# Kernel tuning notes

Hardware: AMD Instinct MI355X
Metric: run time of the kernel (lower is better)

## Reference

```python
import jax, jax.numpy as jnp
import numpy as np

N, XDIM, FACTOR, INTDIM = 1_000_000, 32, 2, 8
HID = XDIM * FACTOR  # 64


def setup_inputs() -> dict:
    key = jax.random.key(0)
    k1, k2, k3, k4, k5, k6 = jax.random.split(key, 6)
    edge_attr3 = jax.random.normal(k1, (N, XDIM), dtype=jnp.float32)
    edge_attr3_old = jax.random.randint(k2, (N, INTDIM), 0, 2).astype(jnp.int32)
    # kaiming-like uniform init (init distribution does not affect reference math)
    bw0 = 1.0 / np.sqrt(XDIM)
    w0 = jax.random.uniform(k3, (INTDIM, XDIM, HID), jnp.float32, -bw0, bw0)
    b0 = jax.random.uniform(k4, (INTDIM, HID), jnp.float32, -bw0, bw0)
    bw1 = 1.0 / np.sqrt(HID)
    w1 = jax.random.uniform(k5, (INTDIM, HID, 1), jnp.float32, -bw1, bw1)
    b1 = jax.random.uniform(k6, (INTDIM, 1), jnp.float32, -bw1, bw1)
    return {"edge_attr3": edge_attr3, "edge_attr3_old": edge_attr3_old,
            "w0": w0, "b0": b0, "w1": w1, "b1": b1}


def reference(edge_attr3, edge_attr3_old, w0, b0, w1, b1):
    # layer 0: per-head GEMM + bias + ReLU -> [n, d, q]
    h = jax.nn.relu(jnp.einsum('np,dpq->ndq', edge_attr3, w0) + b0)
    # layer 1: per-head projection to scalar, then squeeze -> [n, d]
    out = jnp.einsum('ndp,dp->nd', h, w1[:, :, 0]) + b1[:, 0]
    # boolean-mask gather (eager; dynamic output length as in torch out[mask])
    flat_idx = jnp.flatnonzero(edge_attr3_old.astype(bool))
    return out.reshape(-1)[flat_idx]
```

## Files before the change

### kernel.cpp

```cpp
#include <hip/hip_runtime.h>

#define NROWS 1000000
#define NB    3907
#define NT    62500
#define TPB   4
#define NBATCH (NT / TPB)
#define MLP_BLOCKS 1024

typedef __bf16 bf16x8 __attribute__((ext_vector_type(8)));
typedef float  f32x4  __attribute__((ext_vector_type(4)));

__device__ __forceinline__ unsigned cvt_pk_bf16(float lo, float hi) {
  unsigned r;
  asm("v_cvt_pk_bf16_f32 %0, %1, %2" : "=v"(r) : "v"(lo), "v"(hi));
  return r;
}

__global__ __launch_bounds__(256) void count_kernel(
    const int* __restrict__ mask, int* __restrict__ bsum) {
  int tid = threadIdx.x;
  int row = blockIdx.x * 256 + tid;
  int cnt = 0;
  if (row < NROWS) {
    const int4* mp = (const int4*)(mask + (long)row * 8);
    int4 a = mp[0], b = mp[1];
    cnt = (a.x != 0) + (a.y != 0) + (a.z != 0) + (a.w != 0) +
          (b.x != 0) + (b.y != 0) + (b.z != 0) + (b.w != 0);
  }
#pragma unroll
  for (int off = 1; off < 64; off <<= 1) cnt += __shfl_xor(cnt, off);
  __shared__ int ws[4];
  if ((tid & 63) == 0) ws[tid >> 6] = cnt;
  __syncthreads();
  if (tid == 0) bsum[blockIdx.x] = ws[0] + ws[1] + ws[2] + ws[3];
}

__global__ __launch_bounds__(1024) void scan_kernel(
    const int* __restrict__ bsum, int* __restrict__ boff) {
  __shared__ int lds[1024];
  int t = threadIdx.x;
  int i0 = t * 4;
  int c0 = (i0 + 0 < NB) ? bsum[i0 + 0] : 0;
  int c1 = (i0 + 1 < NB) ? bsum[i0 + 1] : 0;
  int c2 = (i0 + 2 < NB) ? bsum[i0 + 2] : 0;
  int c3 = (i0 + 3 < NB) ? bsum[i0 + 3] : 0;
  int s = c0 + c1 + c2 + c3;
  lds[t] = s;
  __syncthreads();
  for (int off = 1; off < 1024; off <<= 1) {
    int v = lds[t];
    int add = (t >= off) ? lds[t - off] : 0;
    __syncthreads();
    lds[t] = v + add;
    __syncthreads();
  }
  int excl = lds[t] - s;
  if (i0 + 0 < NB) boff[i0 + 0] = excl;
  excl += c0;
  if (i0 + 1 < NB) boff[i0 + 1] = excl;
  excl += c1;
  if (i0 + 2 < NB) boff[i0 + 2] = excl;
  excl += c2;
  if (i0 + 3 < NB) boff[i0 + 3] = excl;
}

__global__ __launch_bounds__(256) void expand_kernel(
    const int* __restrict__ mask, const int* __restrict__ boff,
    int* __restrict__ rowinfo) {
  int tid = threadIdx.x;
  int row = blockIdx.x * 256 + tid;
  bool valid = row < NROWS;
  unsigned mb = 0;
  int cnt = 0;
  if (valid) {
    const int4* mp = (const int4*)(mask + (long)row * 8);
    int4 a = mp[0], b = mp[1];
    mb = (unsigned)((a.x != 0) | ((a.y != 0) << 1) | ((a.z != 0) << 2) |
                    ((a.w != 0) << 3) | ((b.x != 0) << 4) | ((b.y != 0) << 5) |
                    ((b.z != 0) << 6) | ((b.w != 0) << 7));
    cnt = __popc(mb);
  }
  int incl = cnt;
#pragma unroll
  for (int off = 1; off < 64; off <<= 1) {
    int v = __shfl_up(incl, off);
    if ((tid & 63) >= off) incl += v;
  }
  __shared__ int wsum[4];
  if ((tid & 63) == 63) wsum[tid >> 6] = incl;
  __syncthreads();
  int w = tid >> 6;
  int wo = 0;
  if (w > 0) wo += wsum[0];
  if (w > 1) wo += wsum[1];
  if (w > 2) wo += wsum[2];
  int pos = boff[blockIdx.x] + wo + (incl - cnt);
  if (valid) rowinfo[row] = (pos << 8) | (int)mb;
}

__global__ __launch_bounds__(256, 2) void mlp_kernel(
    const float* __restrict__ x, const float* __restrict__ w0,
    const float* __restrict__ b0, const float* __restrict__ w1,
    const float* __restrict__ b1, const int* __restrict__ rowinfo,
    float* __restrict__ out) {
  __shared__ __bf16 sA[32 * 64 * 8];
  __shared__ float sB0[512];

  int tid = threadIdx.x;

#pragma unroll
  for (int i = 0; i < 8; ++i) {
    int fi = i * 256 + tid;
    int frag = fi >> 6;
    int lane = fi & 63;
    int d = frag >> 2, qb = frag & 3;
    int q = qb * 16 + (lane & 15);
    int kb = (lane >> 4) * 8;
    bf16x8 v;
#pragma unroll
    for (int j = 0; j < 8; ++j)
      v[j] = (__bf16)w0[d * 2048 + (kb + j) * 64 + q];
    *(bf16x8*)&sA[fi * 8] = v;
  }
  if (tid < 128) *(float4*)&sB0[tid * 4] = *(const float4*)&b0[tid * 4];
  __syncthreads();

  int l = tid & 63;
  int n = l & 15;
  int g = l >> 4;

  bf16x8 w1A, w1B;
  bool ownrow = (n < 8);
#pragma unroll
  for (int j = 0; j < 8; ++j) {
    int off = (j >> 2) * 16 + g * 4 + (j & 3);
    w1A[j] = ownrow ? (__bf16)w1[n * 64 + off]      : (__bf16)0.f;
    w1B[j] = ownrow ? (__bf16)w1[n * 64 + 32 + off] : (__bf16)0.f;
  }
  int4 w1Ai = *(int4*)&w1A;
  int4 w1Bi = *(int4*)&w1B;
  f32x4 b1C;
#pragma unroll
  for (int r = 0; r < 4; ++r) b1C[r] = b1[(g * 4 + r) & 7];

  int w = tid >> 6;
  int wv = blockIdx.x * 4 + w;
  const int W = MLP_BLOCKS * 4;

  for (int b = wv; b < NBATCH; b += W) {
    int t0 = b * TPB;

    bf16x8 xf0, xf1, xf2, xf3;
    {
      const float* xp;
      float4 a, c;
      uint4 ui;
#define LOADX(T, DST)                                              \
      xp = x + (long)((t0 + T) * 16 + n) * 32 + g * 8;             \
      a = *(const float4*)xp; c = *(const float4*)(xp + 4);        \
      ui.x = cvt_pk_bf16(a.x, a.y); ui.y = cvt_pk_bf16(a.z, a.w); \
      ui.z = cvt_pk_bf16(c.x, c.y); ui.w = cvt_pk_bf16(c.z, c.w); \
      DST = *(bf16x8*)&ui;
      LOADX(0, xf0) LOADX(1, xf1) LOADX(2, xf2) LOADX(3, xf3)
#undef LOADX
    }

    f32x4 O0 = b1C, O1 = b1C, O2 = b1C, O3 = b1C;

#pragma unroll 1
    for (int cp = 0; cp < 8; ++cp) {
      bool own = (n == cp);
      int4 z4 = {0, 0, 0, 0};
      int4 A2ai = own ? w1Ai : z4;
      int4 A2bi = own ? w1Bi : z4;
      bf16x8 A2a = *(bf16x8*)&A2ai;
      bf16x8 A2b = *(bf16x8*)&A2bi;
      int fb = cp * 4;
      bf16x8 Aw0 = *(const bf16x8*)&sA[(fb + 0) * 512 + l * 8];
      bf16x8 Aw1 = *(const bf16x8*)&sA[(fb + 1) * 512 + l * 8];
      bf16x8 Aw2 = *(const bf16x8*)&sA[(fb + 2) * 512 + l * 8];
      bf16x8 Aw3 = *(const bf16x8*)&sA[(fb + 3) * 512 + l * 8];
      f32x4 C0 = *(const f32x4*)&sB0[(fb + 0) * 16 + g * 4];
      f32x4 C1 = *(const f32x4*)&sB0[(fb + 1) * 16 + g * 4];
      f32x4 C2 = *(const f32x4*)&sB0[(fb + 2) * 16 + g * 4];
      f32x4 C3 = *(const f32x4*)&sB0[(fb + 3) * 16 + g * 4];

#define TILE(XF, OD) {                                                        \
      f32x4 Da = __builtin_amdgcn_mfma_f32_16x16x32_bf16(Aw0, XF, C0, 0,0,0); \
      f32x4 Db = __builtin_amdgcn_mfma_f32_16x16x32_bf16(Aw1, XF, C1, 0,0,0); \
      uint4 bu;                                                               \
      bu.x = cvt_pk_bf16(fmaxf(Da[0], 0.f), fmaxf(Da[1], 0.f));               \
      bu.y = cvt_pk_bf16(fmaxf(Da[2], 0.f), fmaxf(Da[3], 0.f));               \
      bu.z = cvt_pk_bf16(fmaxf(Db[0], 0.f), fmaxf(Db[1], 0.f));               \
      bu.w = cvt_pk_bf16(fmaxf(Db[2], 0.f), fmaxf(Db[3], 0.f));               \
      bf16x8 B2 = *(bf16x8*)&bu;                                              \
      OD = __builtin_amdgcn_mfma_f32_16x16x32_bf16(A2a, B2, OD, 0, 0, 0);     \
      f32x4 Dc = __builtin_amdgcn_mfma_f32_16x16x32_bf16(Aw2, XF, C2, 0,0,0); \
      f32x4 Dd = __builtin_amdgcn_mfma_f32_16x16x32_bf16(Aw3, XF, C3, 0,0,0); \
      bu.x = cvt_pk_bf16(fmaxf(Dc[0], 0.f), fmaxf(Dc[1], 0.f));               \
      bu.y = cvt_pk_bf16(fmaxf(Dc[2], 0.f), fmaxf(Dc[3], 0.f));               \
      bu.z = cvt_pk_bf16(fmaxf(Dd[0], 0.f), fmaxf(Dd[1], 0.f));               \
      bu.w = cvt_pk_bf16(fmaxf(Dd[2], 0.f), fmaxf(Dd[3], 0.f));               \
      bf16x8 B3 = *(bf16x8*)&bu;                                              \
      OD = __builtin_amdgcn_mfma_f32_16x16x32_bf16(A2b, B3, OD, 0, 0, 0); }
      TILE(xf0, O0) TILE(xf1, O1) TILE(xf2, O2) TILE(xf3, O3)
#undef TILE
    }

    if (g < 2) {
#define EPI(T, OD) {                                                     \
      int row = (t0 + T) * 16 + n;                                       \
      int info = rowinfo[row];                                           \
      unsigned mb = (unsigned)info & 255u;                               \
      int pos = (int)(((unsigned)info) >> 8) +                           \
                (g ? __popc(mb & 0xFu) : 0);                             \
      unsigned nib = (mb >> (g * 4)) & 0xFu;                             \
      if (nib & 1u) { out[pos] = OD[0]; pos++; }                         \
      if (nib & 2u) { out[pos] = OD[1]; pos++; }                         \
      if (nib & 4u) { out[pos] = OD[2]; pos++; }                         \
      if (nib & 8u) { out[pos] = OD[3]; }                                }
      EPI(0, O0) EPI(1, O1) EPI(2, O2) EPI(3, O3)
#undef EPI
    }
  }
}

extern "C" void kernel_launch(void* const* d_in, const int* in_sizes, int n_in,
                              void* d_out, int out_size, void* d_ws, size_t ws_size,
                              hipStream_t stream) {
  const float* x    = (const float*)d_in[0];
  const int*   mask = (const int*)d_in[1];
  const float* w0   = (const float*)d_in[2];
  const float* b0   = (const float*)d_in[3];
  const float* w1   = (const float*)d_in[4];
  const float* b1   = (const float*)d_in[5];
  float* out = (float*)d_out;

  int* bsum    = (int*)d_ws;
  int* boff    = bsum + NB;
  int* rowinfo = boff + NB;

  count_kernel<<<NB, 256, 0, stream>>>(mask, bsum);
  scan_kernel<<<1, 1024, 0, stream>>>(bsum, boff);
  expand_kernel<<<NB, 256, 0, stream>>>(mask, boff, rowinfo);
  mlp_kernel<<<MLP_BLOCKS, 256, 0, stream>>>(x, w0, b0, w1, b1, rowinfo, out);
}
```

Before: 92.25 us.

## Prefetch next batch of x, double-buffer LDS weight fragments, split accumulators

The MLP kernel now loads the next batch's x rows into registers while the current batch computes. It also double-buffers the per-head weight and bias fragments read from LDS across a loop unrolled by two, and splits the second-layer accumulation into two independent MFMA chains that are summed before the scatter. The block count is halved so each wave handles more batches and amortises the prefetch. The aim is to hide global and LDS latency and shorten MFMA dependency chains, at the cost of more registers and fewer resident waves.

```diff
diff --git a/kernel.cpp b/kernel.cpp
--- a/kernel.cpp
+++ b/kernel.cpp
@@ -5,7 +5,8 @@
 #define NT    62500
 #define TPB   4
 #define NBATCH (NT / TPB)
-#define MLP_BLOCKS 1024
+#define MLP_BLOCKS 512
+#define MLP_WAVES (MLP_BLOCKS * 4)
 
 typedef __bf16 bf16x8 __attribute__((ext_vector_type(8)));
 typedef float  f32x4  __attribute__((ext_vector_type(4)));
@@ -107,7 +108,6 @@
   __shared__ float sB0[512];
 
   int tid = threadIdx.x;
-
 #pragma unroll
   for (int i = 0; i < 8; ++i) {
     int fi = i * 256 + tid;
@@ -145,69 +145,122 @@
 
   int w = tid >> 6;
   int wv = blockIdx.x * 4 + w;
-  const int W = MLP_BLOCKS * 4;
+  const int W = MLP_WAVES;
+
+  float4 xa0, xa1, xa2, xa3, xa4, xa5, xa6, xa7;
+  {
+    const float* xp0 = x + (long)((wv * TPB + 0) * 16 + n) * 32 + g * 8;
+    const float* xp1 = x + (long)((wv * TPB + 1) * 16 + n) * 32 + g * 8;
+    const float* xp2 = x + (long)((wv * TPB + 2) * 16 + n) * 32 + g * 8;
+    const float* xp3 = x + (long)((wv * TPB + 3) * 16 + n) * 32 + g * 8;
+    xa0 = *(const float4*)xp0; xa1 = *(const float4*)(xp0 + 4);
+    xa2 = *(const float4*)xp1; xa3 = *(const float4*)(xp1 + 4);
+    xa4 = *(const float4*)xp2; xa5 = *(const float4*)(xp2 + 4);
+    xa6 = *(const float4*)xp3; xa7 = *(const float4*)(xp3 + 4);
+  }
 
   for (int b = wv; b < NBATCH; b += W) {
     int t0 = b * TPB;
 
     bf16x8 xf0, xf1, xf2, xf3;
     {
-      const float* xp;
-      float4 a, c;
       uint4 ui;
-#define LOADX(T, DST)                                              \
-      xp = x + (long)((t0 + T) * 16 + n) * 32 + g * 8;             \
-      a = *(const float4*)xp; c = *(const float4*)(xp + 4);        \
-      ui.x = cvt_pk_bf16(a.x, a.y); ui.y = cvt_pk_bf16(a.z, a.w); \
-      ui.z = cvt_pk_bf16(c.x, c.y); ui.w = cvt_pk_bf16(c.z, c.w); \
+#define CVTX(P, Q, DST)                                            \
+      ui.x = cvt_pk_bf16(P.x, P.y); ui.y = cvt_pk_bf16(P.z, P.w);  \
+      ui.z = cvt_pk_bf16(Q.x, Q.y); ui.w = cvt_pk_bf16(Q.z, Q.w);  \
       DST = *(bf16x8*)&ui;
-      LOADX(0, xf0) LOADX(1, xf1) LOADX(2, xf2) LOADX(3, xf3)
-#undef LOADX
-    }
-
-    f32x4 O0 = b1C, O1 = b1C, O2 = b1C, O3 = b1C;
-
-#pragma unroll 1
-    for (int cp = 0; cp < 8; ++cp) {
-      bool own = (n == cp);
-      int4 z4 = {0, 0, 0, 0};
-      int4 A2ai = own ? w1Ai : z4;
-      int4 A2bi = own ? w1Bi : z4;
-      bf16x8 A2a = *(bf16x8*)&A2ai;
-      bf16x8 A2b = *(bf16x8*)&A2bi;
-      int fb = cp * 4;
-      bf16x8 Aw0 = *(const bf16x8*)&sA[(fb + 0) * 512 + l * 8];
-      bf16x8 Aw1 = *(const bf16x8*)&sA[(fb + 1) * 512 + l * 8];
-      bf16x8 Aw2 = *(const bf16x8*)&sA[(fb + 2) * 512 + l * 8];
-      bf16x8 Aw3 = *(const bf16x8*)&sA[(fb + 3) * 512 + l * 8];
-      f32x4 C0 = *(const f32x4*)&sB0[(fb + 0) * 16 + g * 4];
-      f32x4 C1 = *(const f32x4*)&sB0[(fb + 1) * 16 + g * 4];
-      f32x4 C2 = *(const f32x4*)&sB0[(fb + 2) * 16 + g * 4];
-      f32x4 C3 = *(const f32x4*)&sB0[(fb + 3) * 16 + g * 4];
-
-#define TILE(XF, OD) {                                                        \
-      f32x4 Da = __builtin_amdgcn_mfma_f32_16x16x32_bf16(Aw0, XF, C0, 0,0,0); \
-      f32x4 Db = __builtin_amdgcn_mfma_f32_16x16x32_bf16(Aw1, XF, C1, 0,0,0); \
+      CVTX(xa0, xa1, xf0) CVTX(xa2, xa3, xf1)
+      CVTX(xa4, xa5, xf2) CVTX(xa6, xa7, xf3)
+#undef CVTX
+    }
+
+    {
+      int bn = b + W;
+      if (bn >= NBATCH) bn = b;
+      const float* yp0 = x + (long)((bn * TPB + 0) * 16 + n) * 32 + g * 8;
+      const float* yp1 = x + (long)((bn * TPB + 1) * 16 + n) * 32 + g * 8;
+      const float* yp2 = x + (long)((bn * TPB + 2) * 16 + n) * 32 + g * 8;
+      const float* yp3 = x + (long)((bn * TPB + 3) * 16 + n) * 32 + g * 8;
+      xa0 = *(const float4*)yp0; xa1 = *(const float4*)(yp0 + 4);
+      xa2 = *(const float4*)yp1; xa3 = *(const float4*)(yp1 + 4);
+      xa4 = *(const float4*)yp2; xa5 = *(const float4*)(yp2 + 4);
+      xa6 = *(const float4*)yp3; xa7 = *(const float4*)(yp3 + 4);
+    }
+
+    f32x4 Oa0 = b1C, Oa1 = b1C, Oa2 = b1C, Oa3 = b1C;
+    f32x4 Ob0 = {0.f, 0.f, 0.f, 0.f}, Ob1 = Ob0, Ob2 = Ob0, Ob3 = Ob0;
+
+    bf16x8 fA0 = *(const bf16x8*)&sA[0 * 512 + l * 8];
+    bf16x8 fA1 = *(const bf16x8*)&sA[1 * 512 + l * 8];
+    bf16x8 fA2 = *(const bf16x8*)&sA[2 * 512 + l * 8];
+    bf16x8 fA3 = *(const bf16x8*)&sA[3 * 512 + l * 8];
+    f32x4 cA0 = *(const f32x4*)&sB0[0 * 16 + g * 4];
+    f32x4 cA1 = *(const f32x4*)&sB0[1 * 16 + g * 4];
+    f32x4 cA2 = *(const f32x4*)&sB0[2 * 16 + g * 4];
+    f32x4 cA3 = *(const f32x4*)&sB0[3 * 16 + g * 4];
+
+#define COMPUTE(CP, F0, F1, F2, F3, C0v, C1v, C2v, C3v)                       \
+    {                                                                         \
+      bool own = (n == (CP));                                                 \
+      int4 z4 = {0, 0, 0, 0};                                                 \
+      int4 A2ai = own ? w1Ai : z4;                                            \
+      int4 A2bi = own ? w1Bi : z4;                                            \
+      bf16x8 A2a = *(bf16x8*)&A2ai;                                           \
+      bf16x8 A2b = *(bf16x8*)&A2bi;                                           \
+      TILE(xf0, F0, F1, F2, F3, C0v, C1v, C2v, C3v, Oa0, Ob0)                 \
+      TILE(xf1, F0, F1, F2, F3, C0v, C1v, C2v, C3v, Oa1, Ob1)                 \
+      TILE(xf2, F0, F1, F2, F3, C0v, C1v, C2v, C3v, Oa2, Ob2)                 \
+      TILE(xf3, F0, F1, F2, F3, C0v, C1v, C2v, C3v, Oa3, Ob3)                 \
+    }
+#define TILE(XF, F0, F1, F2, F3, C0v, C1v, C2v, C3v, OA, OB) {                \
+      f32x4 Da = __builtin_amdgcn_mfma_f32_16x16x32_bf16(F0, XF, C0v, 0,0,0); \
+      f32x4 Db = __builtin_amdgcn_mfma_f32_16x16x32_bf16(F1, XF, C1v, 0,0,0); \
       uint4 bu;                                                               \
       bu.x = cvt_pk_bf16(fmaxf(Da[0], 0.f), fmaxf(Da[1], 0.f));               \
       bu.y = cvt_pk_bf16(fmaxf(Da[2], 0.f), fmaxf(Da[3], 0.f));               \
       bu.z = cvt_pk_bf16(fmaxf(Db[0], 0.f), fmaxf(Db[1], 0.f));               \
       bu.w = cvt_pk_bf16(fmaxf(Db[2], 0.f), fmaxf(Db[3], 0.f));               \
       bf16x8 B2 = *(bf16x8*)&bu;                                              \
-      OD = __builtin_amdgcn_mfma_f32_16x16x32_bf16(A2a, B2, OD, 0, 0, 0);     \
-      f32x4 Dc = __builtin_amdgcn_mfma_f32_16x16x32_bf16(Aw2, XF, C2, 0,0,0); \
-      f32x4 Dd = __builtin_amdgcn_mfma_f32_16x16x32_bf16(Aw3, XF, C3, 0,0,0); \
+      OA = __builtin_amdgcn_mfma_f32_16x16x32_bf16(A2a, B2, OA, 0, 0, 0);     \
+      f32x4 Dc = __builtin_amdgcn_mfma_f32_16x16x32_bf16(F2, XF, C2v, 0,0,0); \
+      f32x4 Dd = __builtin_amdgcn_mfma_f32_16x16x32_bf16(F3, XF, C3v, 0,0,0); \
       bu.x = cvt_pk_bf16(fmaxf(Dc[0], 0.f), fmaxf(Dc[1], 0.f));               \
       bu.y = cvt_pk_bf16(fmaxf(Dc[2], 0.f), fmaxf(Dc[3], 0.f));               \
       bu.z = cvt_pk_bf16(fmaxf(Dd[0], 0.f), fmaxf(Dd[1], 0.f));               \
       bu.w = cvt_pk_bf16(fmaxf(Dd[2], 0.f), fmaxf(Dd[3], 0.f));               \
       bf16x8 B3 = *(bf16x8*)&bu;                                              \
-      OD = __builtin_amdgcn_mfma_f32_16x16x32_bf16(A2b, B3, OD, 0, 0, 0); }
-      TILE(xf0, O0) TILE(xf1, O1) TILE(xf2, O2) TILE(xf3, O3)
+      OB = __builtin_amdgcn_mfma_f32_16x16x32_bf16(A2b, B3, OB, 0, 0, 0); }
+
+#pragma unroll 1
+    for (int pp = 0; pp < 4; ++pp) {
+      int cpA = pp * 2, cpB = pp * 2 + 1;
+      int cpN = (pp * 2 + 2) & 7;
+      int fbB = cpB * 4, fbN = cpN * 4;
+      bf16x8 fB0 = *(const bf16x8*)&sA[(fbB + 0) * 512 + l * 8];
+      bf16x8 fB1 = *(const bf16x8*)&sA[(fbB + 1) * 512 + l * 8];
+      bf16x8 fB2 = *(const bf16x8*)&sA[(fbB + 2) * 512 + l * 8];
+      bf16x8 fB3 = *(const bf16x8*)&sA[(fbB + 3) * 512 + l * 8];
+      f32x4 cB0 = *(const f32x4*)&sB0[(fbB + 0) * 16 + g * 4];
+      f32x4 cB1 = *(const f32x4*)&sB0[(fbB + 1) * 16 + g * 4];
+      f32x4 cB2 = *(const f32x4*)&sB0[(fbB + 2) * 16 + g * 4];
+      f32x4 cB3 = *(const f32x4*)&sB0[(fbB + 3) * 16 + g * 4];
+      COMPUTE(cpA, fA0, fA1, fA2, fA3, cA0, cA1, cA2, cA3)
+      fA0 = *(const bf16x8*)&sA[(fbN + 0) * 512 + l * 8];
+      fA1 = *(const bf16x8*)&sA[(fbN + 1) * 512 + l * 8];
+      fA2 = *(const bf16x8*)&sA[(fbN + 2) * 512 + l * 8];
+      fA3 = *(const bf16x8*)&sA[(fbN + 3) * 512 + l * 8];
+      cA0 = *(const f32x4*)&sB0[(fbN + 0) * 16 + g * 4];
+      cA1 = *(const f32x4*)&sB0[(fbN + 1) * 16 + g * 4];
+      cA2 = *(const f32x4*)&sB0[(fbN + 2) * 16 + g * 4];
+      cA3 = *(const f32x4*)&sB0[(fbN + 3) * 16 + g * 4];
+      COMPUTE(cpB, fB0, fB1, fB2, fB3, cB0, cB1, cB2, cB3)
+    }
 #undef TILE
-    }
+#undef COMPUTE
 
     if (g < 2) {
+      f32x4 Os0 = Oa0 + Ob0, Os1 = Oa1 + Ob1;
+      f32x4 Os2 = Oa2 + Ob2, Os3 = Oa3 + Ob3;
 #define EPI(T, OD) {                                                     \
       int row = (t0 + T) * 16 + n;                                       \
       int info = rowinfo[row];                                           \
@@ -219,7 +272,7 @@
       if (nib & 2u) { out[pos] = OD[1]; pos++; }                         \
       if (nib & 4u) { out[pos] = OD[2]; pos++; }                         \
       if (nib & 8u) { out[pos] = OD[3]; }                                }
-      EPI(0, O0) EPI(1, O1) EPI(2, O2) EPI(3, O3)
+      EPI(0, Os0) EPI(1, Os1) EPI(2, Os2) EPI(3, Os3)
 #undef EPI
     }
   }
```

After: 95.59 us. 1.04x slower.

## Assign one head per wave with register-resident weights in 512-thread blocks

Applied to the files above, without the earlier changes.

Reorganizes the MLP kernel so each of eight waves in a 512-thread block handles one head for a shared group of four row tiles. Each wave keeps that head's W0 fragments, bias and W1 in registers, removing the LDS weight staging and the per-head loop. Each wave writes only its head's masked output directly. In exchange, every wave reloads and converts the same x tiles, multiplying x read requests by eight, which relies on cache hits.

```diff
diff --git a/kernel.cpp b/kernel.cpp
--- a/kernel.cpp
+++ b/kernel.cpp
@@ -3,9 +3,8 @@
 #define NROWS 1000000
 #define NB    3907
 #define NT    62500
-#define TPB   4
-#define NBATCH (NT / TPB)
-#define MLP_BLOCKS 1024
+#define GROUPS 15625
+#define MLP_BLOCKS 512
 
 typedef __bf16 bf16x8 __attribute__((ext_vector_type(8)));
 typedef float  f32x4  __attribute__((ext_vector_type(4)));
@@ -98,57 +97,51 @@
   if (valid) rowinfo[row] = (pos << 8) | (int)mb;
 }
 
-__global__ __launch_bounds__(256, 2) void mlp_kernel(
+__global__ __launch_bounds__(512, 4) void mlp_kernel(
     const float* __restrict__ x, const float* __restrict__ w0,
     const float* __restrict__ b0, const float* __restrict__ w1,
     const float* __restrict__ b1, const int* __restrict__ rowinfo,
     float* __restrict__ out) {
-  __shared__ __bf16 sA[32 * 64 * 8];
-  __shared__ float sB0[512];
-
   int tid = threadIdx.x;
-
-#pragma unroll
-  for (int i = 0; i < 8; ++i) {
-    int fi = i * 256 + tid;
-    int frag = fi >> 6;
-    int lane = fi & 63;
-    int d = frag >> 2, qb = frag & 3;
-    int q = qb * 16 + (lane & 15);
-    int kb = (lane >> 4) * 8;
-    bf16x8 v;
-#pragma unroll
-    for (int j = 0; j < 8; ++j)
-      v[j] = (__bf16)w0[d * 2048 + (kb + j) * 64 + q];
-    *(bf16x8*)&sA[fi * 8] = v;
-  }
-  if (tid < 128) *(float4*)&sB0[tid * 4] = *(const float4*)&b0[tid * 4];
-  __syncthreads();
-
+  int hp = tid >> 6;
   int l = tid & 63;
   int n = l & 15;
   int g = l >> 4;
 
-  bf16x8 w1A, w1B;
-  bool ownrow = (n < 8);
+  bf16x8 A0f, A1f, A2f, A3f;
+#define LDA(QB, DST) {                                              \
+    const float* wp = w0 + hp * 2048 + (g * 8) * 64 + QB * 16 + n;  \
+    _Pragma("unroll")                                               \
+    for (int j = 0; j < 8; ++j) DST[j] = (__bf16)wp[j * 64];        }
+  LDA(0, A0f) LDA(1, A1f) LDA(2, A2f) LDA(3, A3f)
+#undef LDA
+  f32x4 C0 = *(const f32x4*)&b0[hp * 64 + 0 * 16 + g * 4];
+  f32x4 C1 = *(const f32x4*)&b0[hp * 64 + 1 * 16 + g * 4];
+  f32x4 C2 = *(const f32x4*)&b0[hp * 64 + 2 * 16 + g * 4];
+  f32x4 C3 = *(const f32x4*)&b0[hp * 64 + 3 * 16 + g * 4];
+  bf16x8 w1a, w1b;
 #pragma unroll
   for (int j = 0; j < 8; ++j) {
     int off = (j >> 2) * 16 + g * 4 + (j & 3);
-    w1A[j] = ownrow ? (__bf16)w1[n * 64 + off]      : (__bf16)0.f;
-    w1B[j] = ownrow ? (__bf16)w1[n * 64 + 32 + off] : (__bf16)0.f;
-  }
-  int4 w1Ai = *(int4*)&w1A;
-  int4 w1Bi = *(int4*)&w1B;
+    w1a[j] = (__bf16)w1[hp * 64 + off];
+    w1b[j] = (__bf16)w1[hp * 64 + 32 + off];
+  }
+  bool own = (n == hp);
+  int4 z4 = {0, 0, 0, 0};
+  int4 tAa = own ? *(int4*)&w1a : z4;
+  int4 tAb = own ? *(int4*)&w1b : z4;
+  bf16x8 A2a = *(bf16x8*)&tAa;
+  bf16x8 A2b = *(bf16x8*)&tAb;
   f32x4 b1C;
 #pragma unroll
   for (int r = 0; r < 4; ++r) b1C[r] = b1[(g * 4 + r) & 7];
 
-  int w = tid >> 6;
-  int wv = blockIdx.x * 4 + w;
-  const int W = MLP_BLOCKS * 4;
-
-  for (int b = wv; b < NBATCH; b += W) {
-    int t0 = b * TPB;
+  int sg = hp >> 2;
+  int sr = hp & 3;
+  unsigned dmask = (1u << hp) - 1u;
+
+  for (int gq = blockIdx.x; gq < GROUPS; gq += MLP_BLOCKS) {
+    int t0 = gq * 4;
 
     bf16x8 xf0, xf1, xf2, xf3;
     {
@@ -158,70 +151,46 @@
 #define LOADX(T, DST)                                              \
       xp = x + (long)((t0 + T) * 16 + n) * 32 + g * 8;             \
       a = *(const float4*)xp; c = *(const float4*)(xp + 4);        \
-      ui.x = cvt_pk_bf16(a.x, a.y); ui.y = cvt_pk_bf16(a.z, a.w); \
-      ui.z = cvt_pk_bf16(c.x, c.y); ui.w = cvt_pk_bf16(c.z, c.w); \
+      ui.x = cvt_pk_bf16(a.x, a.y); ui.y = cvt_pk_bf16(a.z, a.w);  \
+      ui.z = cvt_pk_bf16(c.x, c.y); ui.w = cvt_pk_bf16(c.z, c.w);  \
       DST = *(bf16x8*)&ui;
       LOADX(0, xf0) LOADX(1, xf1) LOADX(2, xf2) LOADX(3, xf3)
 #undef LOADX
     }
 
-    f32x4 O0 = b1C, O1 = b1C, O2 = b1C, O3 = b1C;
-
-#pragma unroll 1
-    for (int cp = 0; cp < 8; ++cp) {
-      bool own = (n == cp);
-      int4 z4 = {0, 0, 0, 0};
-      int4 A2ai = own ? w1Ai : z4;
-      int4 A2bi = own ? w1Bi : z4;
-      bf16x8 A2a = *(bf16x8*)&A2ai;
-      bf16x8 A2b = *(bf16x8*)&A2bi;
-      int fb = cp * 4;
-      bf16x8 Aw0 = *(const bf16x8*)&sA[(fb + 0) * 512 + l * 8];
-      bf16x8 Aw1 = *(const bf16x8*)&sA[(fb + 1) * 512 + l * 8];
-      bf16x8 Aw2 = *(const bf16x8*)&sA[(fb + 2) * 512 + l * 8];
-      bf16x8 Aw3 = *(const bf16x8*)&sA[(fb + 3) * 512 + l * 8];
-      f32x4 C0 = *(const f32x4*)&sB0[(fb + 0) * 16 + g * 4];
-      f32x4 C1 = *(const f32x4*)&sB0[(fb + 1) * 16 + g * 4];
-      f32x4 C2 = *(const f32x4*)&sB0[(fb + 2) * 16 + g * 4];
-      f32x4 C3 = *(const f32x4*)&sB0[(fb + 3) * 16 + g * 4];
-
-#define TILE(XF, OD) {                                                        \
-      f32x4 Da = __builtin_amdgcn_mfma_f32_16x16x32_bf16(Aw0, XF, C0, 0,0,0); \
-      f32x4 Db = __builtin_amdgcn_mfma_f32_16x16x32_bf16(Aw1, XF, C1, 0,0,0); \
+#define TILE(T, XF) {                                                         \
+      f32x4 D0 = __builtin_amdgcn_mfma_f32_16x16x32_bf16(A0f, XF, C0, 0,0,0); \
+      f32x4 D1 = __builtin_amdgcn_mfma_f32_16x16x32_bf16(A1f, XF, C1, 0,0,0); \
+      f32x4 D2 = __builtin_amdgcn_mfma_f32_16x16x32_bf16(A2f, XF, C2, 0,0,0); \
+      f32x4 D3 = __builtin_amdgcn_mfma_f32_16x16x32_bf16(A3f, XF, C3, 0,0,0); \
       uint4 bu;                                                               \
-      bu.x = cvt_pk_bf16(fmaxf(Da[0], 0.f), fmaxf(Da[1], 0.f));               \
-      bu.y = cvt_pk_bf16(fmaxf(Da[2], 0.f), fmaxf(Da[3], 0.f));               \
-      bu.z = cvt_pk_bf16(fmaxf(Db[0], 0.f), fmaxf(Db[1], 0.f));               \
-      bu.w = cvt_pk_bf16(fmaxf(Db[2], 0.f), fmaxf(Db[3], 0.f));               \
+      bu.x = cvt_pk_bf16(fmaxf(D0[0], 0.f), fmaxf(D0[1], 0.f));               \
+      bu.y = cvt_pk_bf16(fmaxf(D0[2], 0.f), fmaxf(D0[3], 0.f));               \
+      bu.z = cvt_pk_bf16(fmaxf(D1[0], 0.f), fmaxf(D1[1], 0.f));               \
+      bu.w = cvt_pk_bf16(fmaxf(D1[2], 0.f), fmaxf(D1[3], 0.f));               \
       bf16x8 B2 = *(bf16x8*)&bu;                                              \
-      OD = __builtin_amdgcn_mfma_f32_16x16x32_bf16(A2a, B2, OD, 0, 0, 0);     \
-      f32x4 Dc = __builtin_amdgcn_mfma_f32_16x16x32_bf16(Aw2, XF, C2, 0,0,0); \
-      f32x4 Dd = __builtin_amdgcn_mfma_f32_16x16x32_bf16(Aw3, XF, C3, 0,0,0); \
-      bu.x = cvt_pk_bf16(fmaxf(Dc[0], 0.f), fmaxf(Dc[1], 0.f));               \
-      bu.y = cvt_pk_bf16(fmaxf(Dc[2], 0.f), fmaxf(Dc[3], 0.f));               \
-      bu.z = cvt_pk_bf16(fmaxf(Dd[0], 0.f), fmaxf(Dd[1], 0.f));               \
-      bu.w = cvt_pk_bf16(fmaxf(Dd[2], 0.f), fmaxf(Dd[3], 0.f));               \
-      bf16x8 B3 = *(bf16x8*)&bu;                                              \
-      OD = __builtin_amdgcn_mfma_f32_16x16x32_bf16(A2b, B3, OD, 0, 0, 0); }
-      TILE(xf0, O0) TILE(xf1, O1) TILE(xf2, O2) TILE(xf3, O3)
+      uint4 bv;                                                               \
+      bv.x = cvt_pk_bf16(fmaxf(D2[0], 0.f), fmaxf(D2[1], 0.f));               \
+      bv.y = cvt_pk_bf16(fmaxf(D2[2], 0.f), fmaxf(D2[3], 0.f));               \
+      bv.z = cvt_pk_bf16(fmaxf(D3[0], 0.f), fmaxf(D3[1], 0.f));               \
+      bv.w = cvt_pk_bf16(fmaxf(D3[2], 0.f), fmaxf(D3[3], 0.f));               \
+      bf16x8 B3 = *(bf16x8*)&bv;                                              \
+      f32x4 O = __builtin_amdgcn_mfma_f32_16x16x32_bf16(A2a, B2, b1C, 0,0,0); \
+      O = __builtin_amdgcn_mfma_f32_16x16x32_bf16(A2b, B3, O, 0, 0, 0);       \
+      if (g == sg) {                                                          \
+        int row = (t0 + T) * 16 + n;                                          \
+        int info = rowinfo[row];                                              \
+        unsigned mb = (unsigned)info & 255u;                                  \
+        if ((mb >> hp) & 1u) {                                                \
+          int pos = (int)(((unsigned)info) >> 8) + __popc(mb & dmask);        \
+          float v = (sr == 0) ? O[0]                                          \
+                  : (sr == 1) ? O[1]                                          \
+                  : (sr == 2) ? O[2] : O[3];                                  \
+          out[pos] = v;                                                       \
+        }                                                                     \
+      }                                                                       }
+    TILE(0, xf0) TILE(1, xf1) TILE(2, xf2) TILE(3, xf3)
 #undef TILE
-    }
-
-    if (g < 2) {
-#define EPI(T, OD) {                                                     \
-      int row = (t0 + T) * 16 + n;                                       \
-      int info = rowinfo[row];                                           \
-      unsigned mb = (unsigned)info & 255u;                               \
-      int pos = (int)(((unsigned)info) >> 8) +                           \
-                (g ? __popc(mb & 0xFu) : 0);                             \
-      unsigned nib = (mb >> (g * 4)) & 0xFu;                             \
-      if (nib & 1u) { out[pos] = OD[0]; pos++; }                         \
-      if (nib & 2u) { out[pos] = OD[1]; pos++; }                         \
-      if (nib & 4u) { out[pos] = OD[2]; pos++; }                         \
-      if (nib & 8u) { out[pos] = OD[3]; }                                }
-      EPI(0, O0) EPI(1, O1) EPI(2, O2) EPI(3, O3)
-#undef EPI
-    }
   }
 }
 
@@ -243,5 +212,5 @@
   count_kernel<<<NB, 256, 0, stream>>>(mask, bsum);
   scan_kernel<<<1, 1024, 0, stream>>>(bsum, boff);
   expand_kernel<<<NB, 256, 0, stream>>>(mask, boff, rowinfo);
-  mlp_kernel<<<MLP_BLOCKS, 256, 0, stream>>>(x, w0, b0, w1, b1, rowinfo, out);
-}
+  mlp_kernel<<<MLP_BLOCKS, 512, 0, stream>>>(x, w0, b0, w1, b1, rowinfo, out);
+}
```

New measurement: 148.6 us. 1.61x slower.
